# Kernel optimization log

Hardware: AMD Instinct MI355X
Metric: run time of the kernel (lower is better)

## Reference

```python
import jax, jax.numpy as jnp
import numpy as np

LMAX = 4
S2_DIM = (LMAX + 1) ** 2                                  # 25: s2 irreps, mul 1 per l
SO3_DIM = sum((2 * l + 1) ** 2 for l in range(LMAX + 1))  # 165: so3 irreps, mul 2l+1 per l
B = 2048
F_S2, F_SO3 = 1, 16
N_S2_KERNEL = 48      # s2_healpix_grid(rec_level=1)
N_SO3_KERNEL = 192    # so3_near_identity_grid()
N_ACT_GRID = 4000     # SO3Activation resolution=10, aspect_ratio=2 -> 20x10x20, flattened
N_EVAL = 4608         # so3_healpix_grid(rec_level=2): 192 pixels x 24 gamma


def setup_inputs() -> dict:
    ks = jax.random.split(jax.random.key(0), 7)
    return {
        "x": jax.random.normal(ks[0], (B, F_S2, S2_DIM), jnp.float32),
        "w_s2": jax.random.normal(ks[1], (F_S2, F_SO3, N_S2_KERNEL), jnp.float32),
        "Y": jax.random.normal(ks[2], (N_S2_KERNEL, S2_DIM), jnp.float32),
        "w_so3": jax.random.normal(ks[3], (F_SO3, 1, N_SO3_KERNEL), jnp.float32),
        "D_kernel": jax.random.normal(ks[4], (N_SO3_KERNEL, SO3_DIM), jnp.float32),
        "D_act": jax.random.normal(ks[5], (N_ACT_GRID, SO3_DIM), jnp.float32),
        "eval_wigners": jax.random.normal(ks[6], (SO3_DIM, N_EVAL), jnp.float32) / np.sqrt(SO3_DIM),
    }


def _s2_to_so3_linear(x, psi):
    # e3nn o3.Linear(s2_irreps -> so3_irreps, f_in, f_out, external weights)
    # x:   [B, f_in, 25]  (mul 1 per degree l)
    # psi: [f_in, f_out, 25] ; column l^2+j is the weight to output-multiplicity j of degree l
    f_in, f_out = psi.shape[0], psi.shape[1]
    out, s = [], 0
    for l in range(LMAX + 1):
        d = 2 * l + 1
        x_l = x[..., s:s + d]                       # [B, f_in, d]
        p_l = psi[..., s:s + d]                     # [f_in, f_out, d] (j = out-mul idx)
        o = jnp.einsum('bxm,xyj->byjm', x_l, p_l) / np.sqrt(f_in)
        out.append(o.reshape(x.shape[0], f_out, d * d))
        s += d
    return jnp.concatenate(out, axis=-1)            # [B, f_out, 165]


def _so3_to_so3_linear(x, psi):
    # e3nn o3.Linear(so3_irreps -> so3_irreps, f_in, f_out, external weights)
    # x:   [B, f_in, 165] ; psi: [f_in, f_out, 165]
    f_in, f_out = psi.shape[0], psi.shape[1]
    out, s = [], 0
    for l in range(LMAX + 1):
        d = 2 * l + 1
        x_l = x[..., s:s + d * d].reshape(x.shape[0], f_in, d, d)   # [B,f_in,u,m]
        p_l = psi[..., s:s + d * d].reshape(f_in, f_out, d, d)      # [f_in,f_out,u,v]
        o = jnp.einsum('bxum,xyuv->byvm', x_l, p_l) / np.sqrt(f_in * d)
        out.append(o.reshape(x.shape[0], f_out, d * d))
        s += d * d
    return jnp.concatenate(out, axis=-1)            # [B, f_out, 165]


def _forward(x, w_s2, Y, w_so3, D_kernel, D_act, eval_wigners):
    # --- S2Convolution: kernel = SH-transform of grid weights, then irrep-wise linear
    psi1 = jnp.einsum('ni,xyn->xyi', Y, w_s2) / np.sqrt(N_S2_KERNEL)     # [1,16,25]
    h = _s2_to_so3_linear(x, psi1)                                        # [B,16,165]
    # --- SO3Activation: Fourier -> SO(3) grid -> relu -> Fourier
    g = jnp.einsum('bfi,gi->bfg', h, D_act) / np.sqrt(SO3_DIM)            # [B,16,4000]
    g = jax.nn.relu(g)
    h = jnp.einsum('bfg,gi->bfi', g, D_act) * (np.sqrt(SO3_DIM) / N_ACT_GRID)
    # --- SO3Convolution
    psi2 = jnp.einsum('ni,xyn->xyi', D_kernel, w_so3) / np.sqrt(N_SO3_KERNEL)  # [16,1,165]
    harmonics = _so3_to_so3_linear(h, psi2)                               # [B,1,165]
    # --- compute_probabilities: matmul with eval Wigner-D basis + softmax over grid
    probs = jax.nn.softmax(jnp.einsum('bfi,ie->be', harmonics, eval_wigners), axis=1)  # [B,4608]
    # --- top-k masking: zero out everything below the 5th-highest prob of sample 0
    fifth = jax.lax.top_k(probs, 5)[0][0, 4]
    probs = jnp.where(probs < fifth, 0.0, probs)
    return harmonics, probs


def reference(x, w_s2, Y, w_so3, D_kernel, D_act, eval_wigners):
    return _forward(x, w_s2, Y, w_so3, D_kernel, D_act, eval_wigners)
```

## Files before the change

kernel.cpp:

```cpp
#include <hip/hip_runtime.h>

typedef short bf16x8 __attribute__((ext_vector_type(8)));
typedef float f32x16 __attribute__((ext_vector_type(16)));
typedef int   i32x4  __attribute__((ext_vector_type(4)));

#define INV_SQRT165 0.07784989441615349f
#define FINAL_SCALE 0.0032113081446662823f
#define ZERO16 ((f32x16){0.f,0.f,0.f,0.f,0.f,0.f,0.f,0.f,0.f,0.f,0.f,0.f,0.f,0.f,0.f,0.f})

__device__ __forceinline__ unsigned short f2bf(float f) {
  unsigned int u = __builtin_bit_cast(unsigned int, f);
  unsigned int r = (u + 0x7FFFu + ((u >> 16) & 1u)) >> 16;
  return (unsigned short)r;
}
__device__ __forceinline__ float bf2f(unsigned short h) {
  unsigned int u = ((unsigned int)h) << 16;
  return __builtin_bit_cast(float, u);
}

__device__ __forceinline__ void gl_lds16(const void* g, void* l) {
  __builtin_amdgcn_global_load_lds(
      (const __attribute__((address_space(1))) unsigned int*)(unsigned long long)g,
      (__attribute__((address_space(3))) unsigned int*)(unsigned int)(unsigned long long)l,
      16, 0, 0);
}

__device__ __forceinline__ void decode_i(int i, int& lv, int& rel) {
  if (i < 1)       { lv = 0; rel = i; }
  else if (i < 10) { lv = 1; rel = i - 1; }
  else if (i < 35) { lv = 2; rel = i - 10; }
  else if (i < 84) { lv = 3; rel = i - 35; }
  else             { lv = 4; rel = i - 84; }
}
__device__ __forceinline__ int divq(int rel, int lv) {
  const int mag[5] = {32768, 10923, 6554, 4682, 3641};
  return (rel * mag[lv]) >> 15;
}

__device__ __forceinline__ int gperm(int p) {
  int a = p & 3, hlp = (p >> 2) & 1, c = p >> 3;
  return ((c >> 1) << 4) + hlp * 8 + ((c & 1) << 2) + a;
}

__global__ __launch_bounds__(256) void prep_k(const float* __restrict__ Da,
                                              const float* __restrict__ ew,
                                              const float* __restrict__ Y,
                                              const float* __restrict__ w_s2,
                                              const float* __restrict__ Dk,
                                              const float* __restrict__ w_so3,
                                              unsigned short* __restrict__ e1pre,
                                              unsigned short* __restrict__ d2pre,
                                              unsigned short* __restrict__ ewpre,
                                              float* __restrict__ psi2) {
  __shared__ __align__(16) unsigned short lds[13824];
  const int tid = threadIdx.x;
  const int l = tid & 63, hl = l >> 5, ln = l & 31;
  if (blockIdx.x < 512) {
    const int ci = blockIdx.x >> 2, yg = blockIdx.x & 3;
    const int g0 = ci * 32;
    float* psi1L = (float*)(lds + 6464);
    for (int e = tid; e < 6400; e += 256) lds[e] = 0;
    for (int e = tid; e < 400; e += 256) {
      int yv = e / 25, iv = e % 25;
      float s = 0.f;
      for (int n = 0; n < 48; n++) s += Y[n * 25 + iv] * w_s2[yv * 48 + n];
      psi1L[e] = s * 0.14433756729740643f;
    }
    __syncthreads();
    int rows = 4000 - g0; if (rows > 32) rows = 32; if (rows < 0) rows = 0;
    int ne = rows * 165;
    for (int e = tid; e < ne; e += 256) {
      int gl_ = e / 165, k = e - gl_ * 165;
      lds[gl_ * 200 + k] = f2bf(Da[g0 * 165 + e]);
    }
    __syncthreads();
    if (yg == 0) {
#pragma unroll
      for (int it = 0; it < 3; it++) {
        int tt = it * 4 + (tid >> 6);
        int nf = tt >> 1, gk = tt & 1;
        unsigned short v[8];
#pragma unroll
        for (int j = 0; j < 8; j++)
          v[j] = lds[(gk * 16 + hl * 8 + j) * 200 + nf * 32 + ln];
        *(i32x4*)(d2pre + ci * 6144 + tt * 512 + l * 8) = *(i32x4*)v;
      }
    }
    for (int yi = 0; yi < 4; yi++) {
      int yy = yg * 4 + yi;
#pragma unroll
      for (int it = 0; it < 4; it++) {
        int idx = it * 256 + tid;
        int kf = idx >> 9, r2 = idx & 511;
        int ll = r2 >> 3, j = r2 & 7;
        int lnn = ll & 31, hll = ll >> 5;
        int k = kf * 16 + hll * 8 + j;
        unsigned short ov = 0;
        if (k < 25) {
          int lv = (k < 1) ? 0 : (k < 4) ? 1 : (k < 9) ? 2 : (k < 16) ? 3 : 4;
          int d = 2 * lv + 1;
          int m = k - lv * lv;
          int off165 = lv * (4 * lv * lv - 1) / 3;
          int gp = gperm(lnn);
          float s = 0.f;
          const float* pr = psi1L + yy * 25 + lv * lv;
          const unsigned short* dr = lds + gp * 200 + off165 + m;
          for (int j2 = 0; j2 < d; j2++) s += pr[j2] * bf2f(dr[j2 * d]);
          ov = f2bf(s * INV_SQRT165);
        }
        e1pre[((yy * 128 + ci) * 2 + kf) * 512 + ll * 8 + j] = ov;
      }
    }
  } else if (blockIdx.x < 584) {
    const int bx2 = blockIdx.x - 512;
    const int n0 = bx2 * 64;
    for (int e = tid; e < 13824; e += 256) lds[e] = 0;
    __syncthreads();
    for (int e = tid; e < 10560; e += 256) {
      int k = e >> 6, n = e & 63;
      lds[k * 72 + n] = f2bf(ew[k * 4608 + n0 + n]);
    }
    __syncthreads();
#pragma unroll
    for (int it = 0; it < 6; it++) {
      int tb = it * 4 + (tid >> 6);
      int nt2 = tb / 12, kf = tb - nt2 * 12;
      unsigned short v[8];
#pragma unroll
      for (int j = 0; j < 8; j++)
        v[j] = lds[(kf * 16 + hl * 8 + j) * 72 + nt2 * 32 + ln];
      *(i32x4*)(ewpre + (bx2 * 2 + nt2) * 6144 + kf * 512 + l * 8) = *(i32x4*)v;
    }
  } else {
    int t = (blockIdx.x - 584) * 256 + tid;
    if (t < 2640) {
      int ch = t / 165, i = t % 165;
      float s = 0.f;
      for (int n = 0; n < 192; n++) s += Dk[n * 165 + i] * w_so3[ch * 192 + n];
      psi2[t] = s * (0.07216878364870323f * FINAL_SCALE);
    }
  }
}

__global__ __launch_bounds__(256, 2) void fused_mlp_k(
    const float* __restrict__ x,
    const unsigned short* __restrict__ e1pre,
    const unsigned short* __restrict__ d2pre,
    unsigned short* __restrict__ part)
{
  __shared__ __align__(16) unsigned char smem[24576];
  const int tid = threadIdx.x;
  const int w = tid >> 6, l = tid & 63;
  const int hl = l >> 5, ln = l & 31;
  const int h = blockIdx.x >> 8;
  const int y = (blockIdx.x >> 4) & 15;
  const int btg = blockIdx.x & 15;
  const int bt = btg * 4 + w;
  const int c0 = h * 63;
  const int cnt = h ? 62 : 63;

  bf16x8 xf[2];
  {
    const float* xr = x + (bt * 32 + ln) * 25;
#pragma unroll
    for (int kf = 0; kf < 2; kf++) {
      unsigned short v[8];
#pragma unroll
      for (int j = 0; j < 8; j++) {
        int k = kf * 16 + hl * 8 + j;
        v[j] = (k < 25) ? f2bf(xr[k]) : (unsigned short)0;
      }
      xf[kf] = *(bf16x8*)v;
    }
  }

  f32x16 o[6];
#pragma unroll
  for (int i = 0; i < 6; i++) o[i] = ZERO16;

  const unsigned short* ebase = e1pre + (y * 128) * 1024;

  bf16x8 eC0 = *(const bf16x8*)(ebase + (c0 * 2 + 0) * 512 + l * 8);
  bf16x8 eC1 = *(const bf16x8*)(ebase + (c0 * 2 + 1) * 512 + l * 8);
#pragma unroll
  for (int i = 0; i < 3; i++) {
    int tb = w * 3 + i;
    gl_lds16(d2pre + c0 * 6144 + tb * 512 + l * 8, smem + tb * 1024);
  }

  for (int ci = 0; ci < cnt; ci++) {
    __syncthreads();
    const unsigned char* cb = smem + (ci & 1) * 12288;
    bf16x8 eN0 = eC0, eN1 = eC1;
    if (ci + 1 < cnt) {
      unsigned char* nb = smem + ((ci + 1) & 1) * 12288;
      const int c = c0 + ci + 1;
#pragma unroll
      for (int i = 0; i < 3; i++) {
        int tb = w * 3 + i;
        gl_lds16(d2pre + c * 6144 + tb * 512 + l * 8, nb + tb * 1024);
      }
      eN0 = *(const bf16x8*)(ebase + (c * 2 + 0) * 512 + l * 8);
      eN1 = *(const bf16x8*)(ebase + (c * 2 + 1) * 512 + l * 8);
    }
    f32x16 s = ZERO16;
    s = __builtin_amdgcn_mfma_f32_32x32x16_bf16(eC0, xf[0], s, 0, 0, 0);
    s = __builtin_amdgcn_mfma_f32_32x32x16_bf16(eC1, xf[1], s, 0, 0, 0);
    unsigned int dw[8];
#pragma unroll
    for (int p = 0; p < 8; p++) {
      float lo = fmaxf(s[2 * p], 0.f), hi = fmaxf(s[2 * p + 1], 0.f);
      asm("v_cvt_pk_bf16_f32 %0, %1, %2" : "=v"(dw[p]) : "v"(lo), "v"(hi));
    }
    i32x4 q0 = (i32x4){(int)dw[0], (int)dw[1], (int)dw[2], (int)dw[3]};
    i32x4 q1 = (i32x4){(int)dw[4], (int)dw[5], (int)dw[6], (int)dw[7]};
    bf16x8 a20 = __builtin_bit_cast(bf16x8, q0);
    bf16x8 a21 = __builtin_bit_cast(bf16x8, q1);
#pragma unroll
    for (int gk = 0; gk < 2; gk++) {
      bf16x8 a2 = gk ? a21 : a20;
#pragma unroll
      for (int nf = 0; nf < 6; nf++) {
        bf16x8 b2 = *(const bf16x8*)(cb + (nf * 2 + gk) * 1024 + l * 16);
        o[nf] = __builtin_amdgcn_mfma_f32_32x32x16_bf16(a2, b2, o[nf], 0, 0, 0);
      }
    }
    eC0 = eN0; eC1 = eN1;
  }

  unsigned short* pp = part + (size_t)((h * 16 + y) * 2048 + bt * 32) * 192;
#pragma unroll
  for (int nf = 0; nf < 6; nf++) {
    int n = nf * 32 + ln;
    if (n < 176) {
#pragma unroll
      for (int r = 0; r < 16; r++) {
        int row = (r & 3) + 8 * (r >> 2) + 4 * hl;
        pp[row * 192 + n] = f2bf(o[nf][r]);
      }
    }
  }
}

__global__ __launch_bounds__(256) void so3_k(const unsigned short* __restrict__ part,
                                             const float* __restrict__ psi2,
                                             float* __restrict__ harm_out,
                                             unsigned short* __restrict__ harmbpre) {
  __shared__ float lds[4 * 16 * 180];
  __shared__ float p2s[2640];
  const int tid = threadIdx.x;
  const int b0 = blockIdx.x * 4;
  for (int e = tid; e < 2640; e += 256) p2s[e] = psi2[e];
  {
    const int ybl = tid >> 2;
    const int yy = ybl & 15, bloc = ybl >> 4;
    const int s = tid & 3;
    const unsigned int* r0 = (const unsigned int*)(part + ((size_t)(0 * 16 + yy) * 2048 + b0 + bloc) * 192);
    const unsigned int* r1 = (const unsigned int*)(part + ((size_t)(1 * 16 + yy) * 2048 + b0 + bloc) * 192);
    float* dst = lds + (bloc * 16 + yy) * 180;
#pragma unroll
    for (int t = 0; t < 22; t++) {
      int d = s * 22 + t;
      if (d < 88) {
        unsigned int u0 = r0[d], u1 = r1[d];
        int n0 = d * 2;
        dst[n0]     = bf2f((unsigned short)(u0 & 0xFFFF)) + bf2f((unsigned short)(u1 & 0xFFFF));
        dst[n0 + 1] = bf2f((unsigned short)(u0 >> 16)) + bf2f((unsigned short)(u1 >> 16));
      }
    }
  }
  __syncthreads();
  for (int jj = tid; jj < 768; jj += 256) {
    int e = (jj * 683) >> 17;
    int i = jj - e * 192;
    int bb = b0 + e;
    unsigned short* hb = harmbpre + (((bb >> 5) * 12 + (i >> 4)) << 9)
                       + ((i >> 3) & 1) * 256 + (bb & 31) * 8 + (i & 7);
    if (i < 165) {
      const float* row0 = lds + e * (16 * 180);
      int lv, rel; decode_i(i, lv, rel);
      int d = 2 * lv + 1;
      int off = i - rel;
      int v = divq(rel, lv), m = rel - v * d;
      float s = 0.f;
      for (int ch = 0; ch < 16; ch++) {
        const float* rw = row0 + ch * 180 + off;
        const float* p2 = p2s + ch * 165 + off;
        for (int u = 0; u < d; u++) s += rw[u * d + m] * p2[u * d + v];
      }
      s *= 0.25f * rsqrtf((float)d);
      harm_out[bb * 165 + i] = s;
      *hb = f2bf(s);
    } else {
      *hb = 0;
    }
  }
}

__global__ __launch_bounds__(64) void eval_k(
    const unsigned short* __restrict__ harmbpre,
    const unsigned short* __restrict__ ewpre,
    float* __restrict__ logits,
    float* __restrict__ logit0)
{
  const int l = threadIdx.x;
  const int hl = l >> 5, ln = l & 31;
  const int mt = blockIdx.y;
  const int n0 = blockIdx.x * 192;

  bf16x8 a[12];
  const short* ap = (const short*)harmbpre + mt * 6144 + l * 8;
#pragma unroll
  for (int kf = 0; kf < 12; kf++) a[kf] = *(const bf16x8*)(ap + kf * 512);

  f32x16 acc[6];
#pragma unroll
  for (int nf = 0; nf < 6; nf++) acc[nf] = ZERO16;

  const short* bp = (const short*)ewpre + (blockIdx.x * 6) * 6144 + l * 8;
#pragma unroll
  for (int kf = 0; kf < 12; kf++) {
#pragma unroll
    for (int nf = 0; nf < 6; nf++) {
      bf16x8 b = *(const bf16x8*)(bp + nf * 6144 + kf * 512);
      acc[nf] = __builtin_amdgcn_mfma_f32_32x32x16_bf16(a[kf], b, acc[nf], 0, 0, 0);
    }
  }
#pragma unroll
  for (int nf = 0; nf < 6; nf++) {
    const int col = n0 + nf * 32 + ln;
#pragma unroll
    for (int r = 0; r < 16; r++) {
      int row = (r & 3) + 8 * (r >> 2) + 4 * hl;
      logits[(mt * 32 + row) * 4608 + col] = acc[nf][r];
    }
  }
  if (mt == 0 && hl == 0) {
#pragma unroll
    for (int nf = 0; nf < 6; nf++) logit0[n0 + nf * 32 + ln] = acc[nf][0];
  }
}

__global__ __launch_bounds__(256) void fifth_k(const float* __restrict__ logit0,
                                               float* __restrict__ fifth) {
  __shared__ float buf[4608];
  __shared__ float sm[4], ss[4];
  __shared__ float wv[4]; __shared__ int wi[4];
  __shared__ float gbest;
  const int tid = threadIdx.x;
  const int l = tid & 63, w = tid >> 6;
  float v[18];
  float mx = -3.4e38f;
#pragma unroll
  for (int i = 0; i < 18; i++) {
    v[i] = logit0[i * 256 + tid];
    buf[i * 256 + tid] = v[i];
    mx = fmaxf(mx, v[i]);
  }
#pragma unroll
  for (int off = 32; off >= 1; off >>= 1) mx = fmaxf(mx, __shfl_xor(mx, off));
  if (l == 0) sm[w] = mx;
  __syncthreads();
  mx = fmaxf(fmaxf(sm[0], sm[1]), fmaxf(sm[2], sm[3]));
  float s = 0.f;
#pragma unroll
  for (int i = 0; i < 18; i++) s += __expf(v[i] - mx);
#pragma unroll
  for (int off = 32; off >= 1; off >>= 1) s += __shfl_xor(s, off);
  if (l == 0) ss[w] = s;
  __syncthreads();
  s = ss[0] + ss[1] + ss[2] + ss[3];
  float inv = 1.f / s;

  float ff = 0.f;
  for (int it = 0; it < 5; it++) {
    float bm = -3.4e38f; int bi = 0;
    for (int i = tid; i < 4608; i += 256) {
      float xx = buf[i];
      if (xx > bm) { bm = xx; bi = i; }
    }
    for (int off = 32; off >= 1; off >>= 1) {
      float ov = __shfl_xor(bm, off); int oi = __shfl_xor(bi, off);
      if (ov > bm) { bm = ov; bi = oi; }
    }
    if (l == 0) { wv[w] = bm; wi[w] = bi; }
    __syncthreads();
    if (tid == 0) {
      float B = wv[0]; int I = wi[0];
      for (int k = 1; k < 4; k++) if (wv[k] > B) { B = wv[k]; I = wi[k]; }
      gbest = B;
      buf[I] = -3.4e38f;
    }
    __syncthreads();
    ff = gbest;
    __syncthreads();
  }
  if (tid == 0) *fifth = __expf(ff - mx) * inv;
}

__global__ __launch_bounds__(256) void smthresh_k(float* __restrict__ probs,
                                                  const float* __restrict__ fifth) {
  float* p = probs + (size_t)blockIdx.x * 4608;
  const int tid = threadIdx.x;
  const int l = tid & 63, w = tid >> 6;
  __shared__ float sm[4], ss[4];
  float v[18];
  float mx = -3.4e38f;
#pragma unroll
  for (int i = 0; i < 18; i++) { v[i] = p[i * 256 + tid]; mx = fmaxf(mx, v[i]); }
#pragma unroll
  for (int off = 32; off >= 1; off >>= 1) mx = fmaxf(mx, __shfl_xor(mx, off));
  if (l == 0) sm[w] = mx;
  __syncthreads();
  mx = fmaxf(fmaxf(sm[0], sm[1]), fmaxf(sm[2], sm[3]));
  float s = 0.f;
#pragma unroll
  for (int i = 0; i < 18; i++) { v[i] = __expf(v[i] - mx); s += v[i]; }
#pragma unroll
  for (int off = 32; off >= 1; off >>= 1) s += __shfl_xor(s, off);
  if (l == 0) ss[w] = s;
  __syncthreads();
  s = ss[0] + ss[1] + ss[2] + ss[3];
  float inv = 1.f / s;
  float t = *fifth;
#pragma unroll
  for (int i = 0; i < 18; i++) {
    float pv = v[i] * inv;
    p[i * 256 + tid] = (pv < t) ? 0.f : pv;
  }
}

extern "C" void kernel_launch(void* const* d_in, const int* in_sizes, int n_in,
                              void* d_out, int out_size, void* d_ws, size_t ws_size,
                              hipStream_t stream) {
  const float* x     = (const float*)d_in[0];
  const float* w_s2  = (const float*)d_in[1];
  const float* Y     = (const float*)d_in[2];
  const float* w_so3 = (const float*)d_in[3];
  const float* Dk    = (const float*)d_in[4];
  const float* Da    = (const float*)d_in[5];
  const float* ew    = (const float*)d_in[6];

  float* out = (float*)d_out;
  float* harm_out = out;
  float* probs    = out + 337920;
  unsigned short* part = (unsigned short*)probs;

  char* ws = (char*)d_ws;
  float* psi2  = (float*)(ws + 0);
  float* fifth = (float*)(ws + 10560);
  unsigned short* e1pre    = (unsigned short*)(ws + 12288);
  unsigned short* d2pre    = (unsigned short*)(ws + 4206592);
  unsigned short* ewpre    = (unsigned short*)(ws + 5779456);
  unsigned short* harmbpre = (unsigned short*)(ws + 7548928);
  float* logit0 = (float*)(ws + 8335360);

  prep_k<<<595, 256, 0, stream>>>(Da, ew, Y, w_s2, Dk, w_so3, e1pre, d2pre, ewpre, psi2);
  fused_mlp_k<<<512, 256, 0, stream>>>(x, e1pre, d2pre, part);
  so3_k<<<512, 256, 0, stream>>>(part, psi2, harm_out, harmbpre);
  eval_k<<<dim3(24, 64), 64, 0, stream>>>(harmbpre, ewpre, probs, logit0);
  fifth_k<<<1, 256, 0, stream>>>(logit0, fifth);
  smthresh_k<<<2048, 256, 0, stream>>>(probs, fifth);
}
```

Before: 215.9 us.

## Split MLP tile per wave into two batch tiles by half of output columns

Each wave now computes two 32-row batch tiles but only half of the 192 output columns, where before it computed one batch tile across all columns. Each LDS-loaded B fragment is reused for two MFMAs and each wave reads half as much of the D2 tile from LDS. The price is that the first-stage GEMM and ReLU are computed twice, once in each of the two waves sharing a batch pair, along with more registers for the second set of inputs. The LDS prefetch assignment is also interleaved across waves.

```diff
diff --git a/kernel.cpp b/kernel.cpp
--- a/kernel.cpp
+++ b/kernel.cpp
@@ -154,14 +154,16 @@
   const int hl = l >> 5, ln = l & 31;
   const int h = blockIdx.x >> 8;
   const int y = (blockIdx.x >> 4) & 15;
-  const int btg = blockIdx.x & 15;
-  const int bt = btg * 4 + w;
+  const int btq = blockIdx.x & 15;
+  const int btp = w & 1, nh = w >> 1;
+  const int bt0 = btq * 4 + btp * 2;
   const int c0 = h * 63;
   const int cnt = h ? 62 : 63;
 
-  bf16x8 xf[2];
-  {
-    const float* xr = x + (bt * 32 + ln) * 25;
+  bf16x8 xf0[2], xf1[2];
+#pragma unroll
+  for (int t = 0; t < 2; t++) {
+    const float* xr = x + ((bt0 + t) * 32 + ln) * 25;
 #pragma unroll
     for (int kf = 0; kf < 2; kf++) {
       unsigned short v[8];
@@ -170,13 +172,13 @@
         int k = kf * 16 + hl * 8 + j;
         v[j] = (k < 25) ? f2bf(xr[k]) : (unsigned short)0;
       }
-      xf[kf] = *(bf16x8*)v;
-    }
-  }
-
-  f32x16 o[6];
-#pragma unroll
-  for (int i = 0; i < 6; i++) o[i] = ZERO16;
+      if (t == 0) xf0[kf] = *(bf16x8*)v; else xf1[kf] = *(bf16x8*)v;
+    }
+  }
+
+  f32x16 o0[3], o1[3];
+#pragma unroll
+  for (int i = 0; i < 3; i++) { o0[i] = ZERO16; o1[i] = ZERO16; }
 
   const unsigned short* ebase = e1pre + (y * 128) * 1024;
 
@@ -184,7 +186,7 @@
   bf16x8 eC1 = *(const bf16x8*)(ebase + (c0 * 2 + 1) * 512 + l * 8);
 #pragma unroll
   for (int i = 0; i < 3; i++) {
-    int tb = w * 3 + i;
+    int tb = w + i * 4;
     gl_lds16(d2pre + c0 * 6144 + tb * 512 + l * 8, smem + tb * 1024);
   }
 
@@ -197,46 +199,55 @@
       const int c = c0 + ci + 1;
 #pragma unroll
       for (int i = 0; i < 3; i++) {
-        int tb = w * 3 + i;
+        int tb = w + i * 4;
         gl_lds16(d2pre + c * 6144 + tb * 512 + l * 8, nb + tb * 1024);
       }
       eN0 = *(const bf16x8*)(ebase + (c * 2 + 0) * 512 + l * 8);
       eN1 = *(const bf16x8*)(ebase + (c * 2 + 1) * 512 + l * 8);
     }
-    f32x16 s = ZERO16;
-    s = __builtin_amdgcn_mfma_f32_32x32x16_bf16(eC0, xf[0], s, 0, 0, 0);
-    s = __builtin_amdgcn_mfma_f32_32x32x16_bf16(eC1, xf[1], s, 0, 0, 0);
-    unsigned int dw[8];
+    f32x16 s0 = ZERO16, s1 = ZERO16;
+    s0 = __builtin_amdgcn_mfma_f32_32x32x16_bf16(eC0, xf0[0], s0, 0, 0, 0);
+    s1 = __builtin_amdgcn_mfma_f32_32x32x16_bf16(eC0, xf1[0], s1, 0, 0, 0);
+    s0 = __builtin_amdgcn_mfma_f32_32x32x16_bf16(eC1, xf0[1], s0, 0, 0, 0);
+    s1 = __builtin_amdgcn_mfma_f32_32x32x16_bf16(eC1, xf1[1], s1, 0, 0, 0);
+    unsigned int dw0[8], dw1[8];
 #pragma unroll
     for (int p = 0; p < 8; p++) {
-      float lo = fmaxf(s[2 * p], 0.f), hi = fmaxf(s[2 * p + 1], 0.f);
-      asm("v_cvt_pk_bf16_f32 %0, %1, %2" : "=v"(dw[p]) : "v"(lo), "v"(hi));
-    }
-    i32x4 q0 = (i32x4){(int)dw[0], (int)dw[1], (int)dw[2], (int)dw[3]};
-    i32x4 q1 = (i32x4){(int)dw[4], (int)dw[5], (int)dw[6], (int)dw[7]};
-    bf16x8 a20 = __builtin_bit_cast(bf16x8, q0);
-    bf16x8 a21 = __builtin_bit_cast(bf16x8, q1);
+      float lo = fmaxf(s0[2 * p], 0.f), hi = fmaxf(s0[2 * p + 1], 0.f);
+      asm("v_cvt_pk_bf16_f32 %0, %1, %2" : "=v"(dw0[p]) : "v"(lo), "v"(hi));
+      float lo1 = fmaxf(s1[2 * p], 0.f), hi1 = fmaxf(s1[2 * p + 1], 0.f);
+      asm("v_cvt_pk_bf16_f32 %0, %1, %2" : "=v"(dw1[p]) : "v"(lo1), "v"(hi1));
+    }
+    bf16x8 a0[2], a1[2];
+    a0[0] = __builtin_bit_cast(bf16x8, (i32x4){(int)dw0[0], (int)dw0[1], (int)dw0[2], (int)dw0[3]});
+    a0[1] = __builtin_bit_cast(bf16x8, (i32x4){(int)dw0[4], (int)dw0[5], (int)dw0[6], (int)dw0[7]});
+    a1[0] = __builtin_bit_cast(bf16x8, (i32x4){(int)dw1[0], (int)dw1[1], (int)dw1[2], (int)dw1[3]});
+    a1[1] = __builtin_bit_cast(bf16x8, (i32x4){(int)dw1[4], (int)dw1[5], (int)dw1[6], (int)dw1[7]});
 #pragma unroll
     for (int gk = 0; gk < 2; gk++) {
-      bf16x8 a2 = gk ? a21 : a20;
-#pragma unroll
-      for (int nf = 0; nf < 6; nf++) {
-        bf16x8 b2 = *(const bf16x8*)(cb + (nf * 2 + gk) * 1024 + l * 16);
-        o[nf] = __builtin_amdgcn_mfma_f32_32x32x16_bf16(a2, b2, o[nf], 0, 0, 0);
+#pragma unroll
+      for (int nf = 0; nf < 3; nf++) {
+        bf16x8 b2 = *(const bf16x8*)(cb + ((nh * 3 + nf) * 2 + gk) * 1024 + l * 16);
+        o0[nf] = __builtin_amdgcn_mfma_f32_32x32x16_bf16(a0[gk], b2, o0[nf], 0, 0, 0);
+        o1[nf] = __builtin_amdgcn_mfma_f32_32x32x16_bf16(a1[gk], b2, o1[nf], 0, 0, 0);
       }
     }
     eC0 = eN0; eC1 = eN1;
   }
 
-  unsigned short* pp = part + (size_t)((h * 16 + y) * 2048 + bt * 32) * 192;
-#pragma unroll
-  for (int nf = 0; nf < 6; nf++) {
-    int n = nf * 32 + ln;
-    if (n < 176) {
-#pragma unroll
-      for (int r = 0; r < 16; r++) {
-        int row = (r & 3) + 8 * (r >> 2) + 4 * hl;
-        pp[row * 192 + n] = f2bf(o[nf][r]);
+#pragma unroll
+  for (int t = 0; t < 2; t++) {
+    unsigned short* pp = part + (size_t)((h * 16 + y) * 2048 + (bt0 + t) * 32) * 192;
+#pragma unroll
+    for (int nf = 0; nf < 3; nf++) {
+      int n = nh * 96 + nf * 32 + ln;
+      if (n < 176) {
+#pragma unroll
+        for (int r = 0; r < 16; r++) {
+          int row = (r & 3) + 8 * (r >> 2) + 4 * hl;
+          float v = t ? o1[nf][r] : o0[nf][r];
+          pp[row * 192 + n] = f2bf(v);
+        }
       }
     }
   }
```

Result: slower. 220.5 us (+2.1%).

## Triple-buffer MLP stages in LDS and stage e1 tiles via global_load_lds

Applied to the files above, without the earlier changes.

The fused MLP loop moves from a double-buffered LDS ring to a three-slot ring. Each slot now also holds the per-channel e1 tiles, fetched asynchronously with global_load_lds instead of direct register loads. The per-iteration __syncthreads is replaced by explicit vmcnt/lgkmcnt waits plus s_barrier, so loads stay two stages ahead of compute. This doubles shared memory per block to 48KB and adds a few redundant padding loads. It relies on the hand-written waitcnt counts matching exactly four loads per stage per thread.

```diff
diff --git a/kernel.cpp b/kernel.cpp
--- a/kernel.cpp
+++ b/kernel.cpp
@@ -148,7 +148,7 @@
     const unsigned short* __restrict__ d2pre,
     unsigned short* __restrict__ part)
 {
-  __shared__ __align__(16) unsigned char smem[24576];
+  __shared__ __align__(16) unsigned char smem[49152];
   const int tid = threadIdx.x;
   const int w = tid >> 6, l = tid & 63;
   const int hl = l >> 5, ln = l & 31;
@@ -180,53 +180,70 @@
 
   const unsigned short* ebase = e1pre + (y * 128) * 1024;
 
-  bf16x8 eC0 = *(const bf16x8*)(ebase + (c0 * 2 + 0) * 512 + l * 8);
-  bf16x8 eC1 = *(const bf16x8*)(ebase + (c0 * 2 + 1) * 512 + l * 8);
-#pragma unroll
-  for (int i = 0; i < 3; i++) {
-    int tb = w * 3 + i;
-    gl_lds16(d2pre + c0 * 6144 + tb * 512 + l * 8, smem + tb * 1024);
-  }
-
-  for (int ci = 0; ci < cnt; ci++) {
-    __syncthreads();
-    const unsigned char* cb = smem + (ci & 1) * 12288;
-    bf16x8 eN0 = eC0, eN1 = eC1;
-    if (ci + 1 < cnt) {
-      unsigned char* nb = smem + ((ci + 1) & 1) * 12288;
-      const int c = c0 + ci + 1;
-#pragma unroll
-      for (int i = 0; i < 3; i++) {
-        int tb = w * 3 + i;
-        gl_lds16(d2pre + c * 6144 + tb * 512 + l * 8, nb + tb * 1024);
-      }
-      eN0 = *(const bf16x8*)(ebase + (c * 2 + 0) * 512 + l * 8);
-      eN1 = *(const bf16x8*)(ebase + (c * 2 + 1) * 512 + l * 8);
-    }
-    f32x16 s = ZERO16;
-    s = __builtin_amdgcn_mfma_f32_32x32x16_bf16(eC0, xf[0], s, 0, 0, 0);
-    s = __builtin_amdgcn_mfma_f32_32x32x16_bf16(eC1, xf[1], s, 0, 0, 0);
-    unsigned int dw[8];
-#pragma unroll
-    for (int p = 0; p < 8; p++) {
-      float lo = fmaxf(s[2 * p], 0.f), hi = fmaxf(s[2 * p + 1], 0.f);
-      asm("v_cvt_pk_bf16_f32 %0, %1, %2" : "=v"(dw[p]) : "v"(lo), "v"(hi));
-    }
-    i32x4 q0 = (i32x4){(int)dw[0], (int)dw[1], (int)dw[2], (int)dw[3]};
-    i32x4 q1 = (i32x4){(int)dw[4], (int)dw[5], (int)dw[6], (int)dw[7]};
-    bf16x8 a20 = __builtin_bit_cast(bf16x8, q0);
-    bf16x8 a21 = __builtin_bit_cast(bf16x8, q1);
-#pragma unroll
-    for (int gk = 0; gk < 2; gk++) {
-      bf16x8 a2 = gk ? a21 : a20;
-#pragma unroll
-      for (int nf = 0; nf < 6; nf++) {
-        bf16x8 b2 = *(const bf16x8*)(cb + (nf * 2 + gk) * 1024 + l * 16);
-        o[nf] = __builtin_amdgcn_mfma_f32_32x32x16_bf16(a2, b2, o[nf], 0, 0, 0);
-      }
-    }
-    eC0 = eN0; eC1 = eN1;
-  }
+#define STAGE(lc, buf) do {                                               \
+    unsigned char* nb_ = smem + (buf) * 16384;                            \
+    const int c_ = c0 + (lc);                                             \
+    _Pragma("unroll")                                                     \
+    for (int i_ = 0; i_ < 4; i_++) {                                      \
+      int tb_ = w * 4 + i_;                                               \
+      int st_ = (tb_ < 14) ? tb_ : (tb_ - 14);                            \
+      const unsigned short* src_ = (st_ < 2)                              \
+          ? ebase + c_ * 1024 + st_ * 512 + l * 8                         \
+          : d2pre + c_ * 6144 + (st_ - 2) * 512 + l * 8;                  \
+      gl_lds16(src_, nb_ + tb_ * 1024);                                   \
+    }                                                                     \
+  } while (0)
+
+#define COMPUTE(cbp) do {                                                  \
+    const unsigned char* cb_ = (cbp);                                      \
+    bf16x8 eC0 = *(const bf16x8*)(cb_ + l * 16);                           \
+    bf16x8 eC1 = *(const bf16x8*)(cb_ + 1024 + l * 16);                    \
+    f32x16 s = ZERO16;                                                     \
+    s = __builtin_amdgcn_mfma_f32_32x32x16_bf16(eC0, xf[0], s, 0, 0, 0);   \
+    s = __builtin_amdgcn_mfma_f32_32x32x16_bf16(eC1, xf[1], s, 0, 0, 0);   \
+    unsigned int dw[8];                                                    \
+    _Pragma("unroll")                                                      \
+    for (int p_ = 0; p_ < 8; p_++) {                                       \
+      float lo = fmaxf(s[2 * p_], 0.f), hi = fmaxf(s[2 * p_ + 1], 0.f);    \
+      asm("v_cvt_pk_bf16_f32 %0, %1, %2" : "=v"(dw[p_]) : "v"(lo), "v"(hi)); \
+    }                                                                      \
+    bf16x8 a20 = __builtin_bit_cast(bf16x8,                                \
+        (i32x4){(int)dw[0], (int)dw[1], (int)dw[2], (int)dw[3]});          \
+    bf16x8 a21 = __builtin_bit_cast(bf16x8,                                \
+        (i32x4){(int)dw[4], (int)dw[5], (int)dw[6], (int)dw[7]});          \
+    _Pragma("unroll")                                                      \
+    for (int gk = 0; gk < 2; gk++) {                                       \
+      bf16x8 a2 = gk ? a21 : a20;                                          \
+      _Pragma("unroll")                                                    \
+      for (int nf = 0; nf < 6; nf++) {                                     \
+        bf16x8 b2 = *(const bf16x8*)(cb_ + 2048 + (nf * 2 + gk) * 1024 + l * 16); \
+        o[nf] = __builtin_amdgcn_mfma_f32_32x32x16_bf16(a2, b2, o[nf], 0, 0, 0);  \
+      }                                                                    \
+    }                                                                      \
+  } while (0)
+
+  STAGE(0, 0);
+  STAGE(1, 1);
+
+  int bufc = 0;
+  for (int ci = 0; ci < cnt - 1; ci++) {
+    asm volatile("s_waitcnt vmcnt(4)" ::: "memory");
+    asm volatile("s_waitcnt lgkmcnt(0)" ::: "memory");
+    __builtin_amdgcn_s_barrier();
+    if (ci + 2 < cnt) {
+      int bn = bufc + 2; if (bn >= 3) bn -= 3;
+      STAGE(ci + 2, bn);
+    }
+    COMPUTE(smem + bufc * 16384);
+    bufc = (bufc == 2) ? 0 : bufc + 1;
+  }
+  asm volatile("s_waitcnt vmcnt(0)" ::: "memory");
+  asm volatile("s_waitcnt lgkmcnt(0)" ::: "memory");
+  __builtin_amdgcn_s_barrier();
+  COMPUTE(smem + bufc * 16384);
+
+#undef STAGE
+#undef COMPUTE
 
   unsigned short* pp = part + (size_t)((h * 16 + y) * 2048 + bt * 32) * 192;
 #pragma unroll
```

After: 214.1 us. Within noise of the previous version (-0.8%).
